# Kernel optimization log

Hardware: AMD Instinct MI355X
Metric: run time of the kernel (lower is better)

Reference implementation:

```python
import jax, jax.numpy as jnp
import numpy as np

N_SRC = 100000
N_EDGES = 1000000
IN_FEATS = 64
N_CLASSES = 64


def setup_inputs() -> dict:
    key = jax.random.key(0)
    k1, k2, k3, k4, k5 = jax.random.split(key, 5)
    x = jax.random.normal(k1, (N_SRC, IN_FEATS), dtype=jnp.float32)
    W_self = jax.random.normal(k2, (IN_FEATS, N_CLASSES), dtype=jnp.float32) / np.sqrt(IN_FEATS)
    W_neigh = jax.random.normal(k3, (IN_FEATS, N_CLASSES), dtype=jnp.float32) / np.sqrt(IN_FEATS)
    b = jnp.zeros((N_CLASSES,), dtype=jnp.float32)
    src = jax.random.randint(k4, (N_EDGES,), 0, N_SRC, dtype=jnp.int32)
    dst = jax.random.randint(k5, (N_EDGES,), 0, N_SRC, dtype=jnp.int32)
    return {"x": x, "W_self": W_self, "W_neigh": W_neigh, "b": b,
            "src": src, "dst": dst, "num_dst": N_SRC}


def reference(x, W_self, W_neigh, b, src, dst, num_dst):
    # SAGEConv 'mean': gather src features along edges, segment-mean into dst,
    # then rst = h_dst @ W_self + h_neigh_mean @ W_neigh + b, followed by relu.
    msgs = x[src]                                                   # [E, F] irregular gather
    summed = jax.ops.segment_sum(msgs, dst, num_segments=num_dst)   # [num_dst, F]
    deg = jax.ops.segment_sum(jnp.ones((src.shape[0],), x.dtype), dst,
                              num_segments=num_dst)                 # [num_dst]
    h_neigh = summed / jnp.maximum(deg, 1.0)[:, None]               # mean (0 for isolated)
    h_dst = x[:num_dst]
    h = h_dst @ W_self + h_neigh @ W_neigh + b
    return jax.nn.relu(h)
```

## Files before the change

### kernel.cpp

```cpp
#include <hip/hip_runtime.h>


constexpr int F = 64;
constexpr int BROWS = 256;
constexpr int MAXNB = 512;
constexpr int CHP = 4096;
constexpr int LDK = 136;
constexpr int QCAP = 4352;
constexpr int LDH = 72;

typedef __attribute__((ext_vector_type(8))) short short8;
typedef __attribute__((ext_vector_type(4))) float float4v;

__device__ inline unsigned short f2bf(float f) {
    union { float f; unsigned u; } c; c.f = f;
    unsigned u = c.u;
    return (unsigned short)((u + 0x7FFFu + ((u >> 16) & 1u)) >> 16);
}
__device__ inline float bf2f(unsigned short h) {
    union { unsigned u; float f; } c; c.u = (unsigned)h << 16;
    return c.f;
}

__global__ __launch_bounds__(256) void k_conv(const float* __restrict__ x,
                                              const float* __restrict__ Ws,
                                              const float* __restrict__ Wn,
                                              unsigned short* __restrict__ xb,
                                              unsigned short* __restrict__ WtG,
                                              const int* __restrict__ dst,
                                              int* __restrict__ cnt,
                                              long n4, int n_edges, int nchunk) {
    __shared__ int hist[MAXNB];
    int t = threadIdx.x;
    long tid = (long)blockIdx.x * 256 + t;
    if (tid < 2 * F * F) {
        int i = (int)tid;
        int n = i & 63, k = i >> 6;
        float v = (k < 64) ? Ws[k * 64 + n] : Wn[(k - 64) * 64 + n];
        WtG[n * 128 + k] = f2bf(v);
    }
    int c = blockIdx.x;
    if (c < nchunk) {
        for (int i = t; i < MAXNB; i += 256) hist[i] = 0;
        __syncthreads();
        int e0 = c * CHP, e1 = min(e0 + CHP, n_edges);
        for (int e = e0 + t; e < e1; e += 256) atomicAdd(&hist[dst[e] >> 8], 1);
        __syncthreads();
        for (int i = t; i < MAXNB; i += 256) cnt[(long)c * MAXNB + i] = hist[i];
    }
    for (long i = tid; i < n4; i += (long)gridDim.x * 256) {
        float4 v = ((const float4*)x)[i];
        ushort4 o;
        o.x = f2bf(v.x); o.y = f2bf(v.y); o.z = f2bf(v.z); o.w = f2bf(v.w);
        ((ushort4*)xb)[i] = o;
    }
}

__global__ __launch_bounds__(512) void k_scanA(int* __restrict__ cnt,
                                               int* __restrict__ btot, int nchunk) {
    int b = (blockIdx.x * 512 + threadIdx.x) >> 6;
    int lane = threadIdx.x & 63;
    if (b >= MAXNB) return;
    int per = (nchunk + 63) / 64;
    int c0 = lane * per;
    int vals[16];
    int lsum = 0;
#pragma unroll
    for (int i = 0; i < 16; ++i) {
        if (i < per) {
            int c = c0 + i;
            int v = (c < nchunk) ? cnt[(long)c * MAXNB + b] : 0;
            vals[i] = v; lsum += v;
        }
    }
    int incl = lsum;
    for (int off = 1; off < 64; off <<= 1) {
        int o = __shfl_up(incl, off);
        if (lane >= off) incl += o;
    }
    int run = incl - lsum;
#pragma unroll
    for (int i = 0; i < 16; ++i) {
        if (i < per) {
            int c = c0 + i;
            if (c < nchunk) { cnt[(long)c * MAXNB + b] = run; run += vals[i]; }
        }
    }
    int tot = __shfl(incl, 63);
    if (lane == 0) btot[b] = tot;
}

__global__ __launch_bounds__(512) void k_scanB(const int* __restrict__ btot,
                                               int* __restrict__ bstart) {
    __shared__ int wtot[8];
    __shared__ int woff[8];
    int t = threadIdx.x;
    int lane = t & 63, wave = t >> 6;
    int v = btot[t];
    int incl = v;
    for (int off = 1; off < 64; off <<= 1) {
        int o = __shfl_up(incl, off);
        if (lane >= off) incl += o;
    }
    if (lane == 63) wtot[wave] = incl;
    __syncthreads();
    if (t == 0) { int s = 0; for (int i = 0; i < 8; ++i) { woff[i] = s; s += wtot[i]; } }
    __syncthreads();
    bstart[t] = incl - v + woff[wave];
    if (t == 511) bstart[MAXNB] = woff[7] + incl;
}

__global__ __launch_bounds__(512) void k_place(const int* __restrict__ src,
                                               const int* __restrict__ dst,
                                               const int* __restrict__ cnt,
                                               const int* __restrict__ bstart,
                                               unsigned* __restrict__ pay, int n_edges) {
    __shared__ int sbp[MAXNB];
    __shared__ int lstart[MAXNB];
    __shared__ int lcur[MAXNB];
    __shared__ unsigned spay[CHP];
    __shared__ int sgpos[CHP];
    __shared__ int wtot[8];
    __shared__ int woff[8];
    int t = threadIdx.x;
    int c = blockIdx.x;
    int e0 = c * CHP, e1 = min(e0 + CHP, n_edges);
    sbp[t] = bstart[t] + cnt[(long)c * MAXNB + t];
    lcur[t] = 0;
    __syncthreads();
    for (int e = e0 + t; e < e1; e += 512) atomicAdd(&lcur[dst[e] >> 8], 1);
    __syncthreads();
    int lane = t & 63, wave = t >> 6;
    int v = lcur[t];
    int incl = v;
    for (int off = 1; off < 64; off <<= 1) {
        int o = __shfl_up(incl, off);
        if (lane >= off) incl += o;
    }
    if (lane == 63) wtot[wave] = incl;
    __syncthreads();
    if (t == 0) { int s = 0; for (int i = 0; i < 8; ++i) { woff[i] = s; s += wtot[i]; } }
    __syncthreads();
    lstart[t] = incl - v + woff[wave];
    lcur[t] = 0;
    __syncthreads();
    for (int e = e0 + t; e < e1; e += 512) {
        int d = dst[e];
        int b = d >> 8;
        int rank = atomicAdd(&lcur[b], 1);
        int idx = lstart[b] + rank;
        spay[idx] = ((unsigned)src[e] << 8) | (unsigned)(d & 255);
        sgpos[idx] = sbp[b] + rank;
    }
    __syncthreads();
    int n = e1 - e0;
    for (int i = t; i < n; i += 512) pay[sgpos[i]] = spay[i];
}

__global__ __launch_bounds__(256) void k_aggemm(const unsigned short* __restrict__ xb,
                                                const unsigned* __restrict__ pay,
                                                const int* __restrict__ bstart,
                                                const unsigned short* __restrict__ WtG,
                                                const float* __restrict__ bias,
                                                float* __restrict__ out,
                                                int num_dst) {
    __shared__ int degs[64];
    __shared__ int rs[64];
    __shared__ int cur[64];
    __shared__ __align__(16) unsigned char upool[64 * LDK * 2];
    __shared__ __align__(16) unsigned short hbt[64 * LDH];
    int* scsr = (int*)upool;
    unsigned short* Wt = (unsigned short*)upool;

    int t = threadIdx.x;
    int blk = blockIdx.x;
    int b = blk >> 2, q = blk & 3;
    int grow0 = b * BROWS + q * 64;
    if (grow0 >= num_dst) return;
    int s0 = bstart[b], s1 = bstart[b + 1];
    int lane = t & 63;
    int wave = t >> 6;

    if (t < 64) degs[t] = 0;
    __syncthreads();
    for (int i = s0 + t; i < s1; i += 256) {
        int row = pay[i] & 255;
        if ((row >> 6) == q) atomicAdd(&degs[row & 63], 1);
    }
    __syncthreads();
    if (t < 64) {
        int v = degs[t];
        int incl = v;
        for (int off = 1; off < 64; off <<= 1) {
            int o = __shfl_up(incl, off);
            if (t >= off) incl += o;
        }
        rs[t] = incl - v;
        cur[t] = incl - v;
    }
    __syncthreads();
    for (int i = s0 + t; i < s1; i += 256) {
        unsigned p = pay[i];
        int row = p & 255;
        if ((row >> 6) == q) {
            int pos = atomicAdd(&cur[row & 63], 1);
            if (pos < QCAP) scsr[pos] = (int)(p >> 8);
        }
    }
    __syncthreads();

    int g = lane >> 3;
    int c8 = (lane & 7) * 8;
#pragma unroll
    for (int batch = 0; batch < 2; ++batch) {
        int rl = wave * 16 + batch * 8 + g;
        int deg = degs[rl];
        int base = rs[rl];
        float acc[8] = {0.f, 0.f, 0.f, 0.f, 0.f, 0.f, 0.f, 0.f};
        for (int k = 0; k < deg; k += 4) {
            int dm = deg - 1;
            int i0 = scsr[base + k];
            int i1 = scsr[base + min(k + 1, dm)];
            int i2 = scsr[base + min(k + 2, dm)];
            int i3 = scsr[base + min(k + 3, dm)];
            short8 u0 = *(const short8*)&xb[(long)i0 * F + c8];
            short8 u1 = *(const short8*)&xb[(long)i1 * F + c8];
            short8 u2 = *(const short8*)&xb[(long)i2 * F + c8];
            short8 u3 = *(const short8*)&xb[(long)i3 * F + c8];
#pragma unroll
            for (int j = 0; j < 8; ++j) acc[j] += bf2f((unsigned short)u0[j]);
            if (k + 1 < deg) {
#pragma unroll
                for (int j = 0; j < 8; ++j) acc[j] += bf2f((unsigned short)u1[j]);
            }
            if (k + 2 < deg) {
#pragma unroll
                for (int j = 0; j < 8; ++j) acc[j] += bf2f((unsigned short)u2[j]);
            }
            if (k + 3 < deg) {
#pragma unroll
                for (int j = 0; j < 8; ++j) acc[j] += bf2f((unsigned short)u3[j]);
            }
        }
        float inv = 1.0f / fmaxf((float)deg, 1.0f);
        short8 o;
#pragma unroll
        for (int j = 0; j < 8; ++j) o[j] = (short)f2bf(acc[j] * inv);
        *(short8*)&hbt[rl * LDH + c8] = o;
    }
    __syncthreads();

    for (int i = t; i < 64 * 16; i += 256) {
        int r = i >> 4, s = i & 15;
        *(short8*)&Wt[r * LDK + s * 8] = *(const short8*)&WtG[r * 128 + s * 8];
    }
    __syncthreads();

    int m = lane & 15;
    int quad = lane >> 4;
    int rowg = grow0 + wave * 16 + m;
    int rx = min(rowg, num_dst - 1);
    const unsigned short* xrow = &xb[(long)rx * F + quad * 8];
    short8 a0 = *(const short8*)(xrow);
    short8 a1 = *(const short8*)(xrow + 32);
    const unsigned short* hrow = &hbt[(wave * 16 + m) * LDH + quad * 8];
    short8 a2 = *(const short8*)(hrow);
    short8 a3 = *(const short8*)(hrow + 32);

    float4v acc[4];
#pragma unroll
    for (int nt = 0; nt < 4; ++nt) acc[nt] = (float4v){0.f, 0.f, 0.f, 0.f};

#pragma unroll
    for (int nt = 0; nt < 4; ++nt) {
        const unsigned short* wrow = &Wt[(nt * 16 + m) * LDK + quad * 8];
        short8 b0 = *(const short8*)(wrow);
        short8 b1 = *(const short8*)(wrow + 32);
        short8 b2 = *(const short8*)(wrow + 64);
        short8 b3 = *(const short8*)(wrow + 96);
        acc[nt] = __builtin_amdgcn_mfma_f32_16x16x32_bf16(a0, b0, acc[nt], 0, 0, 0);
        acc[nt] = __builtin_amdgcn_mfma_f32_16x16x32_bf16(a1, b1, acc[nt], 0, 0, 0);
        acc[nt] = __builtin_amdgcn_mfma_f32_16x16x32_bf16(a2, b2, acc[nt], 0, 0, 0);
        acc[nt] = __builtin_amdgcn_mfma_f32_16x16x32_bf16(a3, b3, acc[nt], 0, 0, 0);
    }

    int gr_base = grow0 + wave * 16 + quad * 4;
#pragma unroll
    for (int nt = 0; nt < 4; ++nt) {
        int col = nt * 16 + m;
        float bv = bias[col];
#pragma unroll
        for (int rg = 0; rg < 4; ++rg) {
            int gg = gr_base + rg;
            if (gg < num_dst) out[(long)gg * F + col] = fmaxf(acc[nt][rg] + bv, 0.0f);
        }
    }
}

__global__ __launch_bounds__(256) void k_scatter(const float* __restrict__ x, const int* __restrict__ src,
                                                 const int* __restrict__ dst, float* __restrict__ summed,
                                                 float* __restrict__ degf, int n_edges) {
    long tid = (long)blockIdx.x * 256 + threadIdx.x;
    int e = (int)(tid >> 6);
    if (e >= n_edges) return;
    int f = threadIdx.x & 63;
    atomicAdd(&summed[(long)dst[e] * F + f], x[(long)src[e] * F + f]);
    if (f == 0) atomicAdd(&degf[dst[e]], 1.0f);
}

__global__ __launch_bounds__(256) void k_gemm_shfl(
    const float* __restrict__ x, const float* __restrict__ Ws, const float* __restrict__ Wn,
    const float* __restrict__ b, const float* __restrict__ degf, float* inout, int num_dst)
{
    __shared__ float Wl[2 * F * F];
    for (int i = threadIdx.x; i < F * F; i += 256) { Wl[i] = Ws[i]; Wl[F * F + i] = Wn[i]; }
    __syncthreads();
    int lane = threadIdx.x & 63;
    int r = (blockIdx.x * 256 + threadIdx.x) >> 6;
    if (r >= num_dst) return;
    float xv = x[(long)r * F + lane];
    float hv = inout[(long)r * F + lane] / fmaxf(degf[r], 1.0f);
    float acc = b[lane];
#pragma unroll
    for (int k = 0; k < F; ++k) {
        acc += __shfl(xv, k) * Wl[k * F + lane];
        acc += __shfl(hv, k) * Wl[(F + k) * F + lane];
    }
    inout[(long)r * F + lane] = fmaxf(acc, 0.0f);
}

extern "C" void kernel_launch(void* const* d_in, const int* in_sizes, int n_in,
                              void* d_out, int out_size, void* d_ws, size_t ws_size,
                              hipStream_t stream) {
    const float* x  = (const float*)d_in[0];
    const float* Ws = (const float*)d_in[1];
    const float* Wn = (const float*)d_in[2];
    const float* b  = (const float*)d_in[3];
    const int* src  = (const int*)d_in[4];
    const int* dst  = (const int*)d_in[5];
    int n_edges = in_sizes[4];
    int num_dst = out_size / F;
    float* out = (float*)d_out;

    int nchunk = (n_edges + CHP - 1) / CHP;
    int nb = (num_dst + BROWS - 1) / BROWS;

    char* ws = (char*)d_ws;
    size_t off = 0;
    auto alloc = [&](size_t bytes) { char* p = ws + off; off = (off + bytes + 255) & ~(size_t)255; return p; };
    unsigned short* xb  = (unsigned short*)alloc((size_t)num_dst * F * 2);
    unsigned* pay       = (unsigned*)alloc((size_t)n_edges * 4);
    unsigned short* WtG = (unsigned short*)alloc(2 * F * F * 2);
    int* cnt            = (int*)alloc((size_t)nchunk * MAXNB * 4);
    int* btot           = (int*)alloc(MAXNB * 4);
    int* bstart         = (int*)alloc((MAXNB + 1) * 4);
    bool big_ws = (off <= ws_size) && (nb <= MAXNB) && (nchunk <= 1024);

    if (big_ws) {
        long n4 = (long)num_dst * F / 4;
        int convgrid = max(2048, nchunk);
        k_conv<<<convgrid, 256, 0, stream>>>(x, Ws, Wn, xb, WtG, dst, cnt, n4, n_edges, nchunk);
        k_scanA<<<(MAXNB * 64 + 511) / 512, 512, 0, stream>>>(cnt, btot, nchunk);
        k_scanB<<<1, 512, 0, stream>>>(btot, bstart);
        k_place<<<nchunk, 512, 0, stream>>>(src, dst, cnt, bstart, pay, n_edges);
        k_aggemm<<<nb * 4, 256, 0, stream>>>(xb, pay, bstart, WtG, b, out, num_dst);
    } else {
        float* degf = (float*)d_ws;
        (void)hipMemsetAsync(d_out, 0, (size_t)out_size * sizeof(float), stream);
        (void)hipMemsetAsync(degf, 0, (size_t)num_dst * sizeof(float), stream);
        long tt = (long)n_edges * 64;
        k_scatter<<<(int)((tt + 255) / 256), 256, 0, stream>>>(x, src, dst, out, degf, n_edges);
        k_gemm_shfl<<<(num_dst + 3) / 4, 256, 0, stream>>>(x, Ws, Wn, b, degf, out, num_dst);
    }
}
```

Baseline: 153.5 us.

## Bucket edges by 64-row destination blocks and drop redundant payload scans

```diff
diff --git a/kernel.cpp b/kernel.cpp
--- a/kernel.cpp
+++ b/kernel.cpp
@@ -2,11 +2,9 @@
 
 
 constexpr int F = 64;
-constexpr int BROWS = 256;
-constexpr int MAXNB = 512;
-constexpr int CHP = 4096;
-constexpr int LDK = 136;
-constexpr int QCAP = 4352;
+constexpr int MAXNB = 2048;
+constexpr int CHP = 2048;
+constexpr int SCAP = 1024;
 constexpr int LDH = 72;
 
 typedef __attribute__((ext_vector_type(8))) short short8;
@@ -44,7 +42,7 @@
         for (int i = t; i < MAXNB; i += 256) hist[i] = 0;
         __syncthreads();
         int e0 = c * CHP, e1 = min(e0 + CHP, n_edges);
-        for (int e = e0 + t; e < e1; e += 256) atomicAdd(&hist[dst[e] >> 8], 1);
+        for (int e = e0 + t; e < e1; e += 256) atomicAdd(&hist[dst[e] >> 6], 1);
         __syncthreads();
         for (int i = t; i < MAXNB; i += 256) cnt[(long)c * MAXNB + i] = hist[i];
     }
@@ -96,8 +94,10 @@
     __shared__ int woff[8];
     int t = threadIdx.x;
     int lane = t & 63, wave = t >> 6;
-    int v = btot[t];
-    int incl = v;
+    int b4 = 4 * t;
+    int v0 = btot[b4], v1 = btot[b4 + 1], v2 = btot[b4 + 2], v3 = btot[b4 + 3];
+    int T = v0 + v1 + v2 + v3;
+    int incl = T;
     for (int off = 1; off < 64; off <<= 1) {
         int o = __shfl_up(incl, off);
         if (lane >= off) incl += o;
@@ -106,8 +106,12 @@
     __syncthreads();
     if (t == 0) { int s = 0; for (int i = 0; i < 8; ++i) { woff[i] = s; s += wtot[i]; } }
     __syncthreads();
-    bstart[t] = incl - v + woff[wave];
-    if (t == 511) bstart[MAXNB] = woff[7] + incl;
+    int base = incl - T + woff[wave];
+    bstart[b4]     = base;
+    bstart[b4 + 1] = base + v0;
+    bstart[b4 + 2] = base + v0 + v1;
+    bstart[b4 + 3] = base + v0 + v1 + v2;
+    if (t == 511) bstart[MAXNB] = base + T;
 }
 
 __global__ __launch_bounds__(512) void k_place(const int* __restrict__ src,
@@ -125,14 +129,31 @@
     int t = threadIdx.x;
     int c = blockIdx.x;
     int e0 = c * CHP, e1 = min(e0 + CHP, n_edges);
-    sbp[t] = bstart[t] + cnt[(long)c * MAXNB + t];
-    lcur[t] = 0;
-    __syncthreads();
-    for (int e = e0 + t; e < e1; e += 512) atomicAdd(&lcur[dst[e] >> 8], 1);
+    for (int i = t; i < MAXNB; i += 512) {
+        sbp[i] = bstart[i] + cnt[(long)c * MAXNB + i];
+        lcur[i] = 0;
+    }
+    __syncthreads();
+    unsigned rpay[4];
+    int rbr[4];
+#pragma unroll
+    for (int j = 0; j < 4; ++j) {
+        int e = e0 + t + j * 512;
+        rbr[j] = -1;
+        if (e < e1) {
+            int d = dst[e];
+            int b = d >> 6;
+            int rank = atomicAdd(&lcur[b], 1);
+            rpay[j] = ((unsigned)src[e] << 6) | (unsigned)(d & 63);
+            rbr[j] = (b << 12) | rank;
+        }
+    }
     __syncthreads();
     int lane = t & 63, wave = t >> 6;
-    int v = lcur[t];
-    int incl = v;
+    int b4 = 4 * t;
+    int v0 = lcur[b4], v1 = lcur[b4 + 1], v2 = lcur[b4 + 2], v3 = lcur[b4 + 3];
+    int T = v0 + v1 + v2 + v3;
+    int incl = T;
     for (int off = 1; off < 64; off <<= 1) {
         int o = __shfl_up(incl, off);
         if (lane >= off) incl += o;
@@ -141,16 +162,20 @@
     __syncthreads();
     if (t == 0) { int s = 0; for (int i = 0; i < 8; ++i) { woff[i] = s; s += wtot[i]; } }
     __syncthreads();
-    lstart[t] = incl - v + woff[wave];
-    lcur[t] = 0;
-    __syncthreads();
-    for (int e = e0 + t; e < e1; e += 512) {
-        int d = dst[e];
-        int b = d >> 8;
-        int rank = atomicAdd(&lcur[b], 1);
-        int idx = lstart[b] + rank;
-        spay[idx] = ((unsigned)src[e] << 8) | (unsigned)(d & 255);
-        sgpos[idx] = sbp[b] + rank;
+    int base = incl - T + woff[wave];
+    lstart[b4]     = base;
+    lstart[b4 + 1] = base + v0;
+    lstart[b4 + 2] = base + v0 + v1;
+    lstart[b4 + 3] = base + v0 + v1 + v2;
+    __syncthreads();
+#pragma unroll
+    for (int j = 0; j < 4; ++j) {
+        if (rbr[j] >= 0) {
+            int b = rbr[j] >> 12, rank = rbr[j] & 4095;
+            int idx = lstart[b] + rank;
+            spay[idx] = rpay[j];
+            sgpos[idx] = sbp[b] + rank;
+        }
     }
     __syncthreads();
     int n = e1 - e0;
@@ -167,25 +192,29 @@
     __shared__ int degs[64];
     __shared__ int rs[64];
     __shared__ int cur[64];
-    __shared__ __align__(16) unsigned char upool[64 * LDK * 2];
+    __shared__ __align__(16) int scsr[SCAP];
     __shared__ __align__(16) unsigned short hbt[64 * LDH];
-    int* scsr = (int*)upool;
-    unsigned short* Wt = (unsigned short*)upool;
-
     int t = threadIdx.x;
-    int blk = blockIdx.x;
-    int b = blk >> 2, q = blk & 3;
-    int grow0 = b * BROWS + q * 64;
+    int qb = blockIdx.x;
+    int grow0 = qb * 64;
     if (grow0 >= num_dst) return;
-    int s0 = bstart[b], s1 = bstart[b + 1];
+    int s0 = bstart[qb], s1 = bstart[qb + 1];
     int lane = t & 63;
     int wave = t >> 6;
 
     if (t < 64) degs[t] = 0;
     __syncthreads();
-    for (int i = s0 + t; i < s1; i += 256) {
-        int row = pay[i] & 255;
-        if ((row >> 6) == q) atomicAdd(&degs[row & 63], 1);
+    int n = s1 - s0;
+    unsigned rp[4];
+#pragma unroll
+    for (int j = 0; j < 4; ++j) {
+        int i = t + j * 256;
+        rp[j] = 0xFFFFFFFFu;
+        if (i < n) {
+            unsigned p = pay[s0 + i];
+            rp[j] = p;
+            atomicAdd(&degs[p & 63], 1);
+        }
     }
     __syncthreads();
     if (t < 64) {
@@ -199,12 +228,11 @@
         cur[t] = incl - v;
     }
     __syncthreads();
-    for (int i = s0 + t; i < s1; i += 256) {
-        unsigned p = pay[i];
-        int row = p & 255;
-        if ((row >> 6) == q) {
-            int pos = atomicAdd(&cur[row & 63], 1);
-            if (pos < QCAP) scsr[pos] = (int)(p >> 8);
+#pragma unroll
+    for (int j = 0; j < 4; ++j) {
+        if (rp[j] != 0xFFFFFFFFu) {
+            int pos = atomicAdd(&cur[rp[j] & 63], 1);
+            if (pos < SCAP) scsr[pos] = (int)(rp[j] >> 6);
         }
     }
     __syncthreads();
@@ -248,13 +276,6 @@
         for (int j = 0; j < 8; ++j) o[j] = (short)f2bf(acc[j] * inv);
         *(short8*)&hbt[rl * LDH + c8] = o;
     }
-    __syncthreads();
-
-    for (int i = t; i < 64 * 16; i += 256) {
-        int r = i >> 4, s = i & 15;
-        *(short8*)&Wt[r * LDK + s * 8] = *(const short8*)&WtG[r * 128 + s * 8];
-    }
-    __syncthreads();
 
     int m = lane & 15;
     int quad = lane >> 4;
@@ -273,7 +294,7 @@
 
 #pragma unroll
     for (int nt = 0; nt < 4; ++nt) {
-        const unsigned short* wrow = &Wt[(nt * 16 + m) * LDK + quad * 8];
+        const unsigned short* wrow = &WtG[(nt * 16 + m) * 128 + quad * 8];
         short8 b0 = *(const short8*)(wrow);
         short8 b1 = *(const short8*)(wrow + 32);
         short8 b2 = *(const short8*)(wrow + 64);
@@ -343,7 +364,7 @@
     float* out = (float*)d_out;
 
     int nchunk = (n_edges + CHP - 1) / CHP;
-    int nb = (num_dst + BROWS - 1) / BROWS;
+    int nb = (num_dst + 63) / 64;
 
     char* ws = (char*)d_ws;
     size_t off = 0;
@@ -363,7 +384,7 @@
         k_scanA<<<(MAXNB * 64 + 511) / 512, 512, 0, stream>>>(cnt, btot, nchunk);
         k_scanB<<<1, 512, 0, stream>>>(btot, bstart);
         k_place<<<nchunk, 512, 0, stream>>>(src, dst, cnt, bstart, pay, n_edges);
-        k_aggemm<<<nb * 4, 256, 0, stream>>>(xb, pay, bstart, WtG, b, out, num_dst);
+        k_aggemm<<<nb, 256, 0, stream>>>(xb, pay, bstart, WtG, b, out, num_dst);
     } else {
         float* degf = (float*)d_ws;
         (void)hipMemsetAsync(d_out, 0, (size_t)out_size * sizeof(float), stream);
```

After: 163.4 us. 1.06x slower.

## Cache edge payloads in registers and widen aggregation blocks to 128 rows

Applied to the files above, without the earlier changes.

```diff
diff --git a/kernel.cpp b/kernel.cpp
--- a/kernel.cpp
+++ b/kernel.cpp
@@ -5,8 +5,7 @@
 constexpr int BROWS = 256;
 constexpr int MAXNB = 512;
 constexpr int CHP = 4096;
-constexpr int LDK = 136;
-constexpr int QCAP = 4352;
+constexpr int SCAP = 2048;
 constexpr int LDH = 72;
 
 typedef __attribute__((ext_vector_type(8))) short short8;
@@ -128,7 +127,20 @@
     sbp[t] = bstart[t] + cnt[(long)c * MAXNB + t];
     lcur[t] = 0;
     __syncthreads();
-    for (int e = e0 + t; e < e1; e += 512) atomicAdd(&lcur[dst[e] >> 8], 1);
+    unsigned rpay[8];
+    int rbr[8];
+#pragma unroll
+    for (int j = 0; j < 8; ++j) {
+        int e = e0 + t + j * 512;
+        rbr[j] = -1;
+        if (e < e1) {
+            int d = dst[e];
+            int b = d >> 8;
+            int rank = atomicAdd(&lcur[b], 1);
+            rpay[j] = ((unsigned)src[e] << 8) | (unsigned)(d & 255);
+            rbr[j] = (b << 12) | rank;
+        }
+    }
     __syncthreads();
     int lane = t & 63, wave = t >> 6;
     int v = lcur[t];
@@ -142,69 +154,99 @@
     if (t == 0) { int s = 0; for (int i = 0; i < 8; ++i) { woff[i] = s; s += wtot[i]; } }
     __syncthreads();
     lstart[t] = incl - v + woff[wave];
-    lcur[t] = 0;
-    __syncthreads();
-    for (int e = e0 + t; e < e1; e += 512) {
-        int d = dst[e];
-        int b = d >> 8;
-        int rank = atomicAdd(&lcur[b], 1);
-        int idx = lstart[b] + rank;
-        spay[idx] = ((unsigned)src[e] << 8) | (unsigned)(d & 255);
-        sgpos[idx] = sbp[b] + rank;
+    __syncthreads();
+#pragma unroll
+    for (int j = 0; j < 8; ++j) {
+        if (rbr[j] >= 0) {
+            int b = rbr[j] >> 12, rank = rbr[j] & 4095;
+            int idx = lstart[b] + rank;
+            spay[idx] = rpay[j];
+            sgpos[idx] = sbp[b] + rank;
+        }
     }
     __syncthreads();
     int n = e1 - e0;
     for (int i = t; i < n; i += 512) pay[sgpos[i]] = spay[i];
 }
 
-__global__ __launch_bounds__(256) void k_aggemm(const unsigned short* __restrict__ xb,
+__global__ __launch_bounds__(512) void k_aggemm(const unsigned short* __restrict__ xb,
                                                 const unsigned* __restrict__ pay,
                                                 const int* __restrict__ bstart,
                                                 const unsigned short* __restrict__ WtG,
                                                 const float* __restrict__ bias,
                                                 float* __restrict__ out,
                                                 int num_dst) {
-    __shared__ int degs[64];
-    __shared__ int rs[64];
-    __shared__ int cur[64];
-    __shared__ __align__(16) unsigned char upool[64 * LDK * 2];
-    __shared__ __align__(16) unsigned short hbt[64 * LDH];
-    int* scsr = (int*)upool;
-    unsigned short* Wt = (unsigned short*)upool;
-
+    __shared__ int degs[128];
+    __shared__ int rs[128];
+    __shared__ int cur[128];
+    __shared__ int wsum[2];
+    __shared__ __align__(16) int scsr[SCAP];
+    __shared__ __align__(16) unsigned short hbt[128 * LDH];
     int t = threadIdx.x;
     int blk = blockIdx.x;
-    int b = blk >> 2, q = blk & 3;
-    int grow0 = b * BROWS + q * 64;
-    if (grow0 >= num_dst) return;
+    int b = blk >> 1, h = blk & 1;
+    int R0 = b * BROWS + h * 128;
+    if (R0 >= num_dst) return;
     int s0 = bstart[b], s1 = bstart[b + 1];
+    int n = s1 - s0;
     int lane = t & 63;
     int wave = t >> 6;
 
-    if (t < 64) degs[t] = 0;
-    __syncthreads();
-    for (int i = s0 + t; i < s1; i += 256) {
-        int row = pay[i] & 255;
-        if ((row >> 6) == q) atomicAdd(&degs[row & 63], 1);
-    }
-    __syncthreads();
-    if (t < 64) {
-        int v = degs[t];
-        int incl = v;
+    if (t < 128) degs[t] = 0;
+    __syncthreads();
+    unsigned rp[8];
+#pragma unroll
+    for (int j = 0; j < 8; ++j) {
+        int i = t + j * 512;
+        rp[j] = 0xFFFFFFFFu;
+        if (i < n) {
+            unsigned p = pay[s0 + i];
+            rp[j] = p;
+            int row = p & 255;
+            if ((row >> 7) == h) atomicAdd(&degs[row & 127], 1);
+        }
+    }
+    for (int i = t + 8 * 512; i < n; i += 512) {
+        unsigned p = pay[s0 + i];
+        int row = p & 255;
+        if ((row >> 7) == h) atomicAdd(&degs[row & 127], 1);
+    }
+    __syncthreads();
+    int sv = 0, sincl = 0;
+    if (t < 128) {
+        sv = degs[t];
+        sincl = sv;
         for (int off = 1; off < 64; off <<= 1) {
-            int o = __shfl_up(incl, off);
-            if (t >= off) incl += o;
-        }
-        rs[t] = incl - v;
-        cur[t] = incl - v;
-    }
-    __syncthreads();
-    for (int i = s0 + t; i < s1; i += 256) {
-        unsigned p = pay[i];
+            int o = __shfl_up(sincl, off);
+            if (lane >= off) sincl += o;
+        }
+        if (lane == 63) wsum[t >> 6] = sincl;
+    }
+    __syncthreads();
+    if (t < 128) {
+        int add = (t >= 64) ? wsum[0] : 0;
+        int ex = sincl - sv + add;
+        rs[t] = ex;
+        cur[t] = ex;
+    }
+    __syncthreads();
+#pragma unroll
+    for (int j = 0; j < 8; ++j) {
+        unsigned p = rp[j];
+        if (p != 0xFFFFFFFFu) {
+            int row = p & 255;
+            if ((row >> 7) == h) {
+                int pos = atomicAdd(&cur[row & 127], 1);
+                if (pos < SCAP) scsr[pos] = (int)(p >> 8);
+            }
+        }
+    }
+    for (int i = t + 8 * 512; i < n; i += 512) {
+        unsigned p = pay[s0 + i];
         int row = p & 255;
-        if ((row >> 6) == q) {
-            int pos = atomicAdd(&cur[row & 63], 1);
-            if (pos < QCAP) scsr[pos] = (int)(p >> 8);
+        if ((row >> 7) == h) {
+            int pos = atomicAdd(&cur[row & 127], 1);
+            if (pos < SCAP) scsr[pos] = (int)(p >> 8);
         }
     }
     __syncthreads();
@@ -248,17 +290,10 @@
         for (int j = 0; j < 8; ++j) o[j] = (short)f2bf(acc[j] * inv);
         *(short8*)&hbt[rl * LDH + c8] = o;
     }
-    __syncthreads();
-
-    for (int i = t; i < 64 * 16; i += 256) {
-        int r = i >> 4, s = i & 15;
-        *(short8*)&Wt[r * LDK + s * 8] = *(const short8*)&WtG[r * 128 + s * 8];
-    }
-    __syncthreads();
 
     int m = lane & 15;
     int quad = lane >> 4;
-    int rowg = grow0 + wave * 16 + m;
+    int rowg = R0 + wave * 16 + m;
     int rx = min(rowg, num_dst - 1);
     const unsigned short* xrow = &xb[(long)rx * F + quad * 8];
     short8 a0 = *(const short8*)(xrow);
@@ -273,7 +308,7 @@
 
 #pragma unroll
     for (int nt = 0; nt < 4; ++nt) {
-        const unsigned short* wrow = &Wt[(nt * 16 + m) * LDK + quad * 8];
+        const unsigned short* wrow = &WtG[(nt * 16 + m) * 128 + quad * 8];
         short8 b0 = *(const short8*)(wrow);
         short8 b1 = *(const short8*)(wrow + 32);
         short8 b2 = *(const short8*)(wrow + 64);
@@ -284,7 +319,7 @@
         acc[nt] = __builtin_amdgcn_mfma_f32_16x16x32_bf16(a3, b3, acc[nt], 0, 0, 0);
     }
 
-    int gr_base = grow0 + wave * 16 + quad * 4;
+    int gr_base = R0 + wave * 16 + quad * 4;
 #pragma unroll
     for (int nt = 0; nt < 4; ++nt) {
         int col = nt * 16 + m;
@@ -363,7 +398,7 @@
         k_scanA<<<(MAXNB * 64 + 511) / 512, 512, 0, stream>>>(cnt, btot, nchunk);
         k_scanB<<<1, 512, 0, stream>>>(btot, bstart);
         k_place<<<nchunk, 512, 0, stream>>>(src, dst, cnt, bstart, pay, n_edges);
-        k_aggemm<<<nb * 4, 256, 0, stream>>>(xb, pay, bstart, WtG, b, out, num_dst);
+        k_aggemm<<<nb * 2, 512, 0, stream>>>(xb, pay, bstart, WtG, b, out, num_dst);
     } else {
         float* degf = (float*)d_ws;
         (void)hipMemsetAsync(d_out, 0, (size_t)out_size * sizeof(float), stream);
```

Result: faster. 146.8 us (-4.3%).
